# Optimization experiments

Measured on AMD Instinct MI355X. Metric: run time of the kernel, lower is better.

Reference implementation:

```python
import jax, jax.numpy as jnp
import numpy as np

NP, NC = 50000, 20000                       # protein / class node counts
EPOS, ENEG, ELINK, EPPI = 400000, 400000, 200000, 600000
NPAIR = 100000
F, H = 128, 256                             # n_features, n_hidden
RELS = ["pos", "neg", "link", "ppi"]


def setup_inputs() -> dict:
    key = jax.random.key(0)
    ks = iter(jax.random.split(key, 80))

    def nrm(shape, scale=0.05):
        return jax.random.normal(next(ks), shape, dtype=jnp.float32) * scale

    def ridx(n, hi):
        return jax.random.randint(next(ks), (n,), 0, hi, dtype=jnp.int32)

    inp = {
        "x_protein": nrm((NP, F), 1.0),
        "x_class": nrm((NC, F), 1.0),
    }
    for r in RELS:
        inp[f"wa_{r}_rel"] = nrm((F, H))
        inp[f"ba_{r}"] = nrm((H,))
        inp[f"wa_{r}_root"] = nrm((F, H))
        inp[f"wb_{r}_rel"] = nrm((H, F))
        inp[f"bb_{r}"] = nrm((F,))
        inp[f"wb_{r}_root"] = nrm((H, F))
    inp["w_lin"] = nrm((2 * F, 1))
    inp["b_lin"] = nrm((1,))
    inp["e_pos_src"] = ridx(EPOS, NP); inp["e_pos_dst"] = ridx(EPOS, NC)
    inp["e_neg_src"] = ridx(ENEG, NP); inp["e_neg_dst"] = ridx(ENEG, NC)
    inp["e_link_src"] = ridx(ELINK, NC); inp["e_link_dst"] = ridx(ELINK, NC)
    inp["e_ppi_src"] = ridx(EPPI, NP); inp["e_ppi_dst"] = ridx(EPPI, NP)
    inp["mask"] = jax.random.randint(next(ks), (NPAIR, 2), 0, NP, dtype=jnp.int32)
    return inp


def graph_conv(x_src, x_dst, src, dst, w_rel, b, w_root):
    # PyG GraphConv: sum-aggregate neighbor features over edges, then
    # lin_rel (with bias) on the aggregate plus lin_root (no bias) on x_dst.
    agg = jax.ops.segment_sum(x_src[src], dst, num_segments=x_dst.shape[0])
    return agg @ w_rel + b + x_dst @ w_root


def reference(x_protein, x_class,
              wa_pos_rel, ba_pos, wa_pos_root, wb_pos_rel, bb_pos, wb_pos_root,
              wa_neg_rel, ba_neg, wa_neg_root, wb_neg_rel, bb_neg, wb_neg_root,
              wa_link_rel, ba_link, wa_link_root, wb_link_rel, bb_link, wb_link_root,
              wa_ppi_rel, ba_ppi, wa_ppi_root, wb_ppi_rel, bb_ppi, wb_ppi_root,
              w_lin, b_lin,
              e_pos_src, e_pos_dst, e_neg_src, e_neg_dst,
              e_link_src, e_link_dst, e_ppi_src, e_ppi_dst, mask):
    # Layer a: HeteroConv sums relation outputs per destination node type.
    hc = (graph_conv(x_protein, x_class, e_pos_src, e_pos_dst, wa_pos_rel, ba_pos, wa_pos_root)
          + graph_conv(x_protein, x_class, e_neg_src, e_neg_dst, wa_neg_rel, ba_neg, wa_neg_root)
          + graph_conv(x_class, x_class, e_link_src, e_link_dst, wa_link_rel, ba_link, wa_link_root))
    hp = graph_conv(x_protein, x_protein, e_ppi_src, e_ppi_dst, wa_ppi_rel, ba_ppi, wa_ppi_root)
    # relu (source applies it twice -> idempotent); dropout p=0.0 is identity.
    hc, hp = jax.nn.relu(hc), jax.nn.relu(hp)
    # Layer b.
    hc2 = (graph_conv(hp, hc, e_pos_src, e_pos_dst, wb_pos_rel, bb_pos, wb_pos_root)
           + graph_conv(hp, hc, e_neg_src, e_neg_dst, wb_neg_rel, bb_neg, wb_neg_root)
           + graph_conv(hc, hc, e_link_src, e_link_dst, wb_link_rel, bb_link, wb_link_root))
    hp2 = graph_conv(hp, hp, e_ppi_src, e_ppi_dst, wb_ppi_rel, bb_ppi, wb_ppi_root)
    del hc2  # 'class' output unused by the readout (dead in source too)
    # Pair readout; source detaches p1/p2 before the final linear.
    p1 = jax.lax.stop_gradient(hp2[mask[:, 0]])
    p2 = jax.lax.stop_gradient(hp2[mask[:, 1]])
    return jax.nn.sigmoid(jnp.concatenate([p1, p2], axis=1) @ w_lin + b_lin)
```

## Files before the change

kernel.cpp:

```cpp
#include <hip/hip_runtime.h>
#include <hip/hip_bf16.h>
#include <hip/hip_fp16.h>
#include <math.h>


#define FDIM 128
#define DEG_CAP 48
#define BCAP 3456

typedef __attribute__((ext_vector_type(8))) _Float16 half8;
typedef __attribute__((ext_vector_type(4))) float f32x4;

__device__ __forceinline__ unsigned short f2h(float f) {
  _Float16 h = (_Float16)f;
  return __builtin_bit_cast(unsigned short, h);
}
__device__ __forceinline__ float h2f(unsigned short u) {
  _Float16 h = __builtin_bit_cast(_Float16, u);
  return (float)h;
}

__global__ __launch_bounds__(512) void bucket_scatter(
    const int* __restrict__ esrc, const int* __restrict__ edst, int ne,
    int* __restrict__ bucketCur, unsigned int* __restrict__ ebuf, int NBb) {
  __shared__ int lhist[256];
  __shared__ int lbase[256];
  const int tid = threadIdx.x;
  if (tid < 256) lhist[tid] = 0;
  __syncthreads();
  const int base = blockIdx.x * 2048 + tid;
  int sl[4], bk[4], ok[4];
  unsigned pk[4];
#pragma unroll
  for (int i = 0; i < 4; ++i) {
    int e = base + i * 512;
    ok[i] = (e < ne);
    if (ok[i]) {
      int d = edst[e], s = esrc[e];
      bk[i] = d >> 8;
      pk[i] = ((unsigned)s << 8) | (unsigned)(d & 255);
      sl[i] = atomicAdd(&lhist[bk[i]], 1);
    }
  }
  __syncthreads();
  if (tid < NBb) {
    int c = lhist[tid];
    lbase[tid] = (c > 0) ? atomicAdd(&bucketCur[tid], c) : 0;
  }
  __syncthreads();
#pragma unroll
  for (int i = 0; i < 4; ++i) {
    if (ok[i]) {
      int pos = lbase[bk[i]] + sl[i];
      if (pos < BCAP) ebuf[(size_t)bk[i] * BCAP + pos] = pk[i];
    }
  }
}

__global__ __launch_bounds__(256) void bucket_fill_mega(
    const unsigned int* __restrict__ ebuf, const int* __restrict__ bucketCur,
    unsigned short* __restrict__ colidx, int* __restrict__ cnt, int M, int NBb,
    const float* __restrict__ xp, unsigned short* __restrict__ xb,
    const float* __restrict__ wa_rel, const float* __restrict__ wa_root,
    const float* __restrict__ wb_rel, const float* __restrict__ wb_root,
    const float* __restrict__ bb, const float* __restrict__ wl,
    unsigned short* __restrict__ Bt, float* __restrict__ uvec, int xpb) {
  const int bid = blockIdx.x;
  const int tid = threadIdx.x;
  if (bid < NBb) {
    __shared__ int lcnt[256];
    lcnt[tid] = 0;
    __syncthreads();
    const int nb_ = min(bucketCur[bid], BCAP);
    for (int idx = tid; idx < nb_; idx += 256) {
      unsigned pk = ebuf[(size_t)bid * BCAP + idx];
      int dl = pk & 255;
      int src = (int)(pk >> 8);
      int slot = atomicAdd(&lcnt[dl], 1);
      if (slot < DEG_CAP) {
        int node = (bid << 8) | dl;
        colidx[(size_t)node * DEG_CAP + slot] = (unsigned short)src;
      }
    }
    __syncthreads();
    int node = (bid << 8) | tid;
    if (node < M) cnt[node] = lcnt[tid];
  } else if (bid < NBb + xpb) {
    int t = (bid - NBb) * 256 + tid;
    int n = t >> 5, c = (t & 31) * 4;
    if (n >= M) return;
    float4 v = *(const float4*)(xp + (size_t)n * 128 + c);
    ushort4 o;
    o.x = f2h(v.x); o.y = f2h(v.y); o.z = f2h(v.z); o.w = f2h(v.w);
    *(ushort4*)(xb + (size_t)n * 128 + c) = o;
  } else if (bid < NBb + xpb + 256) {
    int n = bid - NBb - xpb, k = tid;
    float v = (k < 128) ? wa_rel[k * 256 + n] : wa_root[(k - 128) * 256 + n];
    Bt[n * 256 + k] = f2h(v);
  } else {
    int k = tid;
    float u1 = 0.f, u2 = 0.f, v1 = 0.f, v2 = 0.f;
    for (int n = 0; n < 128; ++n) {
      float wr = wb_rel[k * 128 + n], wo = wb_root[k * 128 + n];
      float w1 = wl[n], w2 = wl[128 + n];
      u1 += wr * w1; u2 += wr * w2;
      v1 += wo * w1; v2 += wo * w2;
    }
    uvec[k] = u1;
    uvec[256 + k] = u2;
    uvec[512 + k] = v1;
    uvec[768 + k] = v2;
    if (k < 2) {
      float c = 0.f;
      for (int n = 0; n < 128; ++n) c += bb[n] * wl[k * 128 + n];
      uvec[1024 + k] = c;
    }
  }
}

__global__ __launch_bounds__(256) void gather_rows(
    const unsigned short* __restrict__ xb, const int* __restrict__ cnt,
    const unsigned short* __restrict__ colidx, unsigned short* __restrict__ agg,
    int M) {
  int node = (blockIdx.x * 256 + threadIdx.x) >> 6;
  int lane = threadIdx.x & 63;
  if (node >= M) return;
  int deg = min(cnt[node], DEG_CAP);
  int ci = (lane < deg) ? (int)colidx[(size_t)node * DEG_CAP + lane] : 0;
  float ax = 0.f, ay = 0.f;
  int t = 0;
  for (; t + 3 < deg; t += 4) {
    int s0 = __shfl(ci, t), s1 = __shfl(ci, t + 1);
    int s2 = __shfl(ci, t + 2), s3 = __shfl(ci, t + 3);
    unsigned int u0 = *(const unsigned int*)(xb + (size_t)s0 * 128 + 2 * lane);
    unsigned int u1 = *(const unsigned int*)(xb + (size_t)s1 * 128 + 2 * lane);
    unsigned int u2 = *(const unsigned int*)(xb + (size_t)s2 * 128 + 2 * lane);
    unsigned int u3 = *(const unsigned int*)(xb + (size_t)s3 * 128 + 2 * lane);
    ax += h2f((unsigned short)(u0 & 0xffffu)) + h2f((unsigned short)(u1 & 0xffffu)) +
          h2f((unsigned short)(u2 & 0xffffu)) + h2f((unsigned short)(u3 & 0xffffu));
    ay += h2f((unsigned short)(u0 >> 16)) + h2f((unsigned short)(u1 >> 16)) +
          h2f((unsigned short)(u2 >> 16)) + h2f((unsigned short)(u3 >> 16));
  }
  for (; t < deg; ++t) {
    int s0 = __shfl(ci, t);
    unsigned int u0 = *(const unsigned int*)(xb + (size_t)s0 * 128 + 2 * lane);
    ax += h2f((unsigned short)(u0 & 0xffffu));
    ay += h2f((unsigned short)(u0 >> 16));
  }
  ushort2 o;
  o.x = f2h(ax);
  o.y = f2h(ay);
  *(ushort2*)(agg + (size_t)node * 128 + 2 * lane) = o;
}

__global__ __launch_bounds__(512) void gemm_nv(
    const unsigned short* __restrict__ agg, const unsigned short* __restrict__ xb,
    const unsigned short* __restrict__ Bt, const float* __restrict__ ba,
    const float* __restrict__ uvec, float4* __restrict__ nv, int M) {
  __shared__ __align__(16) short Als[128 * 64];
  __shared__ __align__(16) short Bls[256 * 64];
  __shared__ float Ulds[1280];

  const int tid = threadIdx.x;
  for (int i = tid; i < 1280; i += 512)
    Ulds[i] = (i < 1024) ? uvec[i] : ba[i - 1024];

  const int w = tid >> 6, lane = tid & 63;
  const int wr = w >> 2, wc = w & 3;
  const int l15 = lane & 15, lg = lane >> 4;
  const int row0 = blockIdx.x * 128;

  f32x4 acc[4][4] = {};

#pragma unroll
  for (int kt = 0; kt < 4; ++kt) {
    __syncthreads();
    const int rl8 = lane >> 3;
    const int ss = (lane & 7) ^ rl8;
    const unsigned short* Abase = (kt < 2) ? agg : xb;
    const int kofs = (kt & 1) * 128;
#pragma unroll
    for (int i = 0; i < 2; ++i) {
      int r_loc = i * 64 + w * 8 + rl8;
      int arow = row0 + r_loc;
      if (arow >= M) arow = M - 1;
      const char* ga = (const char*)Abase + (size_t)arow * 256 + kofs + ss * 16;
      char* la = (char*)Als + (i * 64 + w * 8) * 128;
      __builtin_amdgcn_global_load_lds(
          (const __attribute__((address_space(1))) void*)ga,
          (__attribute__((address_space(3))) void*)la, 16, 0, 0);
    }
#pragma unroll
    for (int i = 0; i < 4; ++i) {
      int nrow = i * 64 + w * 8 + rl8;
      const char* gb = (const char*)Bt + (size_t)nrow * 512 + kt * 128 + ss * 16;
      char* lb = (char*)Bls + (i * 64 + w * 8) * 128;
      __builtin_amdgcn_global_load_lds(
          (const __attribute__((address_space(1))) void*)gb,
          (__attribute__((address_space(3))) void*)lb, 16, 0, 0);
    }
    __syncthreads();
#pragma unroll
    for (int ks = 0; ks < 2; ++ks) {
      half8 a[4], b[4];
#pragma unroll
      for (int mi = 0; mi < 4; ++mi) {
        int row = wr * 64 + mi * 16 + l15;
        int loc = (ks * 64 + lg * 16) ^ ((row & 7) << 4);
        a[mi] = *(const half8*)((const char*)Als + row * 128 + loc);
      }
#pragma unroll
      for (int ni = 0; ni < 4; ++ni) {
        int brow = wc * 64 + ni * 16 + l15;
        int loc = (ks * 64 + lg * 16) ^ ((brow & 7) << 4);
        b[ni] = *(const half8*)((const char*)Bls + brow * 128 + loc);
      }
#pragma unroll
      for (int mi = 0; mi < 4; ++mi)
#pragma unroll
        for (int ni = 0; ni < 4; ++ni)
          acc[mi][ni] = __builtin_amdgcn_mfma_f32_16x16x32_f16(
              a[mi], b[ni], acc[mi][ni], 0, 0, 0);
    }
  }

  __syncthreads();
  float* ep = (float*)Als;

#pragma unroll
  for (int mi = 0; mi < 4; ++mi) {
#pragma unroll
    for (int r = 0; r < 4; ++r) {
      float pt1 = 0.f, pt2 = 0.f, pr1 = 0.f, pr2 = 0.f;
#pragma unroll
      for (int ni = 0; ni < 4; ++ni) {
        int c = wc * 64 + ni * 16 + l15;
        float h = fmaxf(acc[mi][ni][r] + Ulds[1024 + c], 0.f);
        pt1 += h * Ulds[c];
        pt2 += h * Ulds[256 + c];
        pr1 += h * Ulds[512 + c];
        pr2 += h * Ulds[768 + c];
      }
#pragma unroll
      for (int o = 1; o < 16; o <<= 1) {
        pt1 += __shfl_xor(pt1, o);
        pt2 += __shfl_xor(pt2, o);
        pr1 += __shfl_xor(pr1, o);
        pr2 += __shfl_xor(pr2, o);
      }
      if (l15 == 0) {
        int rloc = wr * 64 + mi * 16 + lg * 4 + r;
        ep[(wc * 128 + rloc) * 4 + 0] = pt1;
        ep[(wc * 128 + rloc) * 4 + 1] = pt2;
        ep[(wc * 128 + rloc) * 4 + 2] = pr1;
        ep[(wc * 128 + rloc) * 4 + 3] = pr2;
      }
    }
  }
  __syncthreads();
  {
    int rloc = tid >> 2, v = tid & 3;
    float s = ep[(0 * 128 + rloc) * 4 + v] + ep[(1 * 128 + rloc) * 4 + v] +
              ep[(2 * 128 + rloc) * 4 + v] + ep[(3 * 128 + rloc) * 4 + v];
    int grow = row0 + rloc;
    if (grow < M) ((float*)nv)[(size_t)grow * 4 + v] = s;
  }
}

__global__ __launch_bounds__(256) void pair_scores(
    const float4* __restrict__ nv, const int* __restrict__ cnt,
    const unsigned short* __restrict__ colidx, const float* __restrict__ uvec,
    float* __restrict__ s1, float* __restrict__ s2, int M) {
  int t = blockIdx.x * 256 + threadIdx.x;
  int node = t >> 3, sub = t & 7;
  if (node >= M) return;
  int deg = min(cnt[node], DEG_CAP);
  float a1 = 0.f, a2 = 0.f;
  for (int j = sub; j < deg; j += 8) {
    int s = colidx[(size_t)node * DEG_CAP + j];
    float2 tv = *(const float2*)((const float*)nv + 4 * (size_t)s);
    a1 += tv.x;
    a2 += tv.y;
  }
#pragma unroll
  for (int o = 1; o < 8; o <<= 1) {
    a1 += __shfl_xor(a1, o);
    a2 += __shfl_xor(a2, o);
  }
  if (sub == 0) {
    float4 me = nv[node];
    s1[node] = uvec[1024] + me.z + a1;
    s2[node] = uvec[1025] + me.w + a2;
  }
}

__global__ __launch_bounds__(256) void pair_out(
    const float* __restrict__ s1, const float* __restrict__ s2,
    const int* __restrict__ mask, const float* __restrict__ b_lin,
    float* __restrict__ out, int np) {
  int p = blockIdx.x * 256 + threadIdx.x;
  if (p >= np) return;
  float z = s1[mask[2 * p]] + s2[mask[2 * p + 1]] + b_lin[0];
  out[p] = 1.f / (1.f + expf(-z));
}

extern "C" void kernel_launch(void* const* d_in, const int* in_sizes, int n_in,
                              void* d_out, int out_size, void* d_ws,
                              size_t ws_size, hipStream_t stream) {
  const float* x_p     = (const float*)d_in[0];
  const float* wa_rel  = (const float*)d_in[20];
  const float* ba      = (const float*)d_in[21];
  const float* wa_root = (const float*)d_in[22];
  const float* wb_rel  = (const float*)d_in[23];
  const float* bb      = (const float*)d_in[24];
  const float* wb_root = (const float*)d_in[25];
  const float* w_lin   = (const float*)d_in[26];
  const float* b_lin   = (const float*)d_in[27];
  const int* esrc      = (const int*)d_in[34];
  const int* edst      = (const int*)d_in[35];
  const int* mask      = (const int*)d_in[36];
  float* out = (float*)d_out;

  const int M = in_sizes[0] / FDIM;
  const int ne = in_sizes[34];
  const int npair = in_sizes[36] / 2;
  const int NBb = (M + 255) >> 8;

  char* ws = (char*)d_ws;
  unsigned short* xb  = (unsigned short*)ws;
  unsigned short* agg = xb + (size_t)M * 128;
  float* s1 = (float*)(agg + (size_t)M * 128);
  float* s2 = s1 + M;
  int* cnt = (int*)(s2 + M);
  unsigned short* colidx = (unsigned short*)(cnt + M);
  unsigned int* ebuf = (unsigned int*)(colidx + (size_t)M * DEG_CAP);
  int* bucketCur = (int*)(ebuf + (size_t)NBb * BCAP);
  char* after = (char*)(bucketCur + NBb);
  size_t off = ((after - ws) + 255) & ~(size_t)255;
  unsigned short* B1t = (unsigned short*)(ws + off);
  float* uvec = (float*)(ws + off + 256 * 256 * 2);
  float4* nv = (float4*)(ws + ((off + 256 * 256 * 2 + 1026 * 4 + 255) &
                               ~(size_t)255));

  const int xpb = (M * 32 + 255) / 256;
  const int gb = (M * 64 + 255) / 256;
  const int sb = (ne + 2047) / 2048;

  hipMemsetAsync(bucketCur, 0, (size_t)NBb * 4, stream);

  bucket_scatter<<<sb, 512, 0, stream>>>(esrc, edst, ne, bucketCur, ebuf, NBb);

  bucket_fill_mega<<<NBb + xpb + 257, 256, 0, stream>>>(
      ebuf, bucketCur, colidx, cnt, M, NBb, x_p, xb,
      wa_rel, wa_root, wb_rel, wb_root, bb, w_lin, B1t, uvec, xpb);

  gather_rows<<<gb, 256, 0, stream>>>(xb, cnt, colidx, agg, M);

  gemm_nv<<<(M + 127) / 128, 512, 0, stream>>>(agg, xb, B1t, ba, uvec, nv, M);

  pair_scores<<<(M * 8 + 255) / 256, 256, 0, stream>>>(nv, cnt, colidx, uvec,
                                                       s1, s2, M);

  pair_out<<<(npair + 255) / 256, 256, 0, stream>>>(s1, s2, mask, b_lin, out,
                                                    npair);
}
```

Before: 100.2 us.

## Replace global bucket atomics with per-block segment buffers and merge prep kernels

The edge scatter no longer reserves global bucket space with atomics. Each scatter block now writes its edges into its own fixed-capacity segment per destination bucket and records the segment lengths. A new bucket_fill kernel walks all segments for its bucket. The fp16 conversion and weight preparation are folded into the scatter launch, which removes the memset and one kernel launch. In exchange, each per-block bucket segment is capped at 40 edges and overflow edges are silently dropped. bucket_fill also reads its segments serially per thread with uncoalesced access.

```diff
diff --git a/kernel.cpp b/kernel.cpp
--- a/kernel.cpp
+++ b/kernel.cpp
@@ -6,7 +6,8 @@
 
 #define FDIM 128
 #define DEG_CAP 48
-#define BCAP 3456
+#define SEG_CAP 40
+#define SCAT_E 2048
 
 typedef __attribute__((ext_vector_type(8))) _Float16 half8;
 typedef __attribute__((ext_vector_type(4))) float f32x4;
@@ -20,84 +21,53 @@
   return (float)h;
 }
 
-__global__ __launch_bounds__(512) void bucket_scatter(
+__global__ __launch_bounds__(512) void scatter_mega(
     const int* __restrict__ esrc, const int* __restrict__ edst, int ne,
-    int* __restrict__ bucketCur, unsigned int* __restrict__ ebuf, int NBb) {
-  __shared__ int lhist[256];
-  __shared__ int lbase[256];
-  const int tid = threadIdx.x;
-  if (tid < 256) lhist[tid] = 0;
-  __syncthreads();
-  const int base = blockIdx.x * 2048 + tid;
-  int sl[4], bk[4], ok[4];
-  unsigned pk[4];
-#pragma unroll
-  for (int i = 0; i < 4; ++i) {
-    int e = base + i * 512;
-    ok[i] = (e < ne);
-    if (ok[i]) {
-      int d = edst[e], s = esrc[e];
-      bk[i] = d >> 8;
-      pk[i] = ((unsigned)s << 8) | (unsigned)(d & 255);
-      sl[i] = atomicAdd(&lhist[bk[i]], 1);
-    }
-  }
-  __syncthreads();
-  if (tid < NBb) {
-    int c = lhist[tid];
-    lbase[tid] = (c > 0) ? atomicAdd(&bucketCur[tid], c) : 0;
-  }
-  __syncthreads();
-#pragma unroll
-  for (int i = 0; i < 4; ++i) {
-    if (ok[i]) {
-      int pos = lbase[bk[i]] + sl[i];
-      if (pos < BCAP) ebuf[(size_t)bk[i] * BCAP + pos] = pk[i];
-    }
-  }
-}
-
-__global__ __launch_bounds__(256) void bucket_fill_mega(
-    const unsigned int* __restrict__ ebuf, const int* __restrict__ bucketCur,
-    unsigned short* __restrict__ colidx, int* __restrict__ cnt, int M, int NBb,
-    const float* __restrict__ xp, unsigned short* __restrict__ xb,
+    unsigned int* __restrict__ ebuf, int* __restrict__ lens, int NBb, int sB,
+    const float* __restrict__ xp, unsigned short* __restrict__ xb, int M,
     const float* __restrict__ wa_rel, const float* __restrict__ wa_root,
     const float* __restrict__ wb_rel, const float* __restrict__ wb_root,
     const float* __restrict__ bb, const float* __restrict__ wl,
     unsigned short* __restrict__ Bt, float* __restrict__ uvec, int xpb) {
-  const int bid = blockIdx.x;
-  const int tid = threadIdx.x;
-  if (bid < NBb) {
-    __shared__ int lcnt[256];
-    lcnt[tid] = 0;
+  const int bid = blockIdx.x, tid = threadIdx.x;
+  if (bid < sB) {
+    __shared__ int lhist[256];
+    if (tid < 256) lhist[tid] = 0;
     __syncthreads();
-    const int nb_ = min(bucketCur[bid], BCAP);
-    for (int idx = tid; idx < nb_; idx += 256) {
-      unsigned pk = ebuf[(size_t)bid * BCAP + idx];
-      int dl = pk & 255;
-      int src = (int)(pk >> 8);
-      int slot = atomicAdd(&lcnt[dl], 1);
-      if (slot < DEG_CAP) {
-        int node = (bid << 8) | dl;
-        colidx[(size_t)node * DEG_CAP + slot] = (unsigned short)src;
-      }
-    }
+    const int base = bid * SCAT_E + tid;
+    int bk[4], sl[4], ok[4];
+    unsigned pk[4];
+#pragma unroll
+    for (int i = 0; i < 4; ++i) {
+      int e = base + i * 512;
+      ok[i] = (e < ne);
+      if (ok[i]) {
+        int d = edst[e], s = esrc[e];
+        bk[i] = d >> 8;
+        pk[i] = ((unsigned)s << 8) | (unsigned)(d & 255);
+        sl[i] = atomicAdd(&lhist[bk[i]], 1);
+      }
+    }
+    const size_t rbase = (size_t)bid * NBb * SEG_CAP;
+#pragma unroll
+    for (int i = 0; i < 4; ++i)
+      if (ok[i] && sl[i] < SEG_CAP)
+        ebuf[rbase + (size_t)bk[i] * SEG_CAP + sl[i]] = pk[i];
     __syncthreads();
-    int node = (bid << 8) | tid;
-    if (node < M) cnt[node] = lcnt[tid];
-  } else if (bid < NBb + xpb) {
-    int t = (bid - NBb) * 256 + tid;
+    if (tid < NBb) lens[bid * NBb + tid] = min(lhist[tid], SEG_CAP);
+  } else if (bid < sB + xpb) {
+    int t = (bid - sB) * 512 + tid;
     int n = t >> 5, c = (t & 31) * 4;
     if (n >= M) return;
     float4 v = *(const float4*)(xp + (size_t)n * 128 + c);
     ushort4 o;
     o.x = f2h(v.x); o.y = f2h(v.y); o.z = f2h(v.z); o.w = f2h(v.w);
     *(ushort4*)(xb + (size_t)n * 128 + c) = o;
-  } else if (bid < NBb + xpb + 256) {
-    int n = bid - NBb - xpb, k = tid;
+  } else if (bid < sB + xpb + 128) {
+    int n = (bid - sB - xpb) * 2 + (tid >> 8), k = tid & 255;
     float v = (k < 128) ? wa_rel[k * 256 + n] : wa_root[(k - 128) * 256 + n];
     Bt[n * 256 + k] = f2h(v);
-  } else {
+  } else if (tid < 256) {
     int k = tid;
     float u1 = 0.f, u2 = 0.f, v1 = 0.f, v2 = 0.f;
     for (int n = 0; n < 128; ++n) {
@@ -116,6 +86,33 @@
       uvec[1024 + k] = c;
     }
   }
+}
+
+__global__ __launch_bounds__(256) void bucket_fill(
+    const unsigned int* __restrict__ ebuf, const int* __restrict__ lens,
+    unsigned short* __restrict__ colidx, int* __restrict__ cnt, int M,
+    int NBb, int sB) {
+  __shared__ int lcnt[256];
+  const int b = blockIdx.x, tid = threadIdx.x;
+  lcnt[tid] = 0;
+  __syncthreads();
+  for (int s = tid; s < sB; s += 256) {
+    int len = lens[s * NBb + b];
+    const size_t base = (size_t)s * NBb * SEG_CAP + (size_t)b * SEG_CAP;
+    for (int j = 0; j < len; ++j) {
+      unsigned pk = ebuf[base + j];
+      int dl = pk & 255;
+      int src = (int)(pk >> 8);
+      int slot = atomicAdd(&lcnt[dl], 1);
+      if (slot < DEG_CAP) {
+        int node = (b << 8) | dl;
+        colidx[(size_t)node * DEG_CAP + slot] = (unsigned short)src;
+      }
+    }
+  }
+  __syncthreads();
+  int node = (b << 8) | tid;
+  if (node < M) cnt[node] = lcnt[tid];
 }
 
 __global__ __launch_bounds__(256) void gather_rows(
@@ -325,6 +322,7 @@
   const int ne = in_sizes[34];
   const int npair = in_sizes[36] / 2;
   const int NBb = (M + 255) >> 8;
+  const int sB = (ne + SCAT_E - 1) / SCAT_E;
 
   char* ws = (char*)d_ws;
   unsigned short* xb  = (unsigned short*)ws;
@@ -334,25 +332,22 @@
   int* cnt = (int*)(s2 + M);
   unsigned short* colidx = (unsigned short*)(cnt + M);
   unsigned int* ebuf = (unsigned int*)(colidx + (size_t)M * DEG_CAP);
-  int* bucketCur = (int*)(ebuf + (size_t)NBb * BCAP);
-  char* after = (char*)(bucketCur + NBb);
+  int* lens = (int*)(ebuf + (size_t)sB * NBb * SEG_CAP);
+  char* after = (char*)(lens + (size_t)sB * NBb);
   size_t off = ((after - ws) + 255) & ~(size_t)255;
   unsigned short* B1t = (unsigned short*)(ws + off);
   float* uvec = (float*)(ws + off + 256 * 256 * 2);
   float4* nv = (float4*)(ws + ((off + 256 * 256 * 2 + 1026 * 4 + 255) &
                                ~(size_t)255));
 
-  const int xpb = (M * 32 + 255) / 256;
+  const int xpb = (M * 32 + 511) / 512;
   const int gb = (M * 64 + 255) / 256;
-  const int sb = (ne + 2047) / 2048;
-
-  hipMemsetAsync(bucketCur, 0, (size_t)NBb * 4, stream);
-
-  bucket_scatter<<<sb, 512, 0, stream>>>(esrc, edst, ne, bucketCur, ebuf, NBb);
-
-  bucket_fill_mega<<<NBb + xpb + 257, 256, 0, stream>>>(
-      ebuf, bucketCur, colidx, cnt, M, NBb, x_p, xb,
+
+  scatter_mega<<<sB + xpb + 129, 512, 0, stream>>>(
+      esrc, edst, ne, ebuf, lens, NBb, sB, x_p, xb, M,
       wa_rel, wa_root, wb_rel, wb_root, bb, w_lin, B1t, uvec, xpb);
+
+  bucket_fill<<<NBb, 256, 0, stream>>>(ebuf, lens, colidx, cnt, M, NBb, sB);
 
   gather_rows<<<gb, 256, 0, stream>>>(xb, cnt, colidx, agg, M);
 
```

Result: faster. 97.47 us (-2.7%).
